# Kernel tuning notes

Measured on AMD Instinct MI355X. Metric: run time of the kernel, lower is better.

## Reference

```python
import jax, jax.numpy as jnp
import numpy as np

B, L, T, D, H, DH = 8, 1024, 1024, 768, 12, 64
SPATIAL_DIM = 5


def setup_inputs() -> dict:
    key = jax.random.key(0)
    ks = jax.random.split(key, 12)
    scale = 1.0 / np.sqrt(D)
    inp = {
        "q": jax.random.normal(ks[0], (B, L, D), dtype=jnp.float32),
        "k": jax.random.normal(ks[1], (B, T, D), dtype=jnp.float32),
        "v": jax.random.normal(ks[2], (B, T, D), dtype=jnp.float32),
        "pairwise_locs": jax.random.normal(ks[3], (B, L, T, SPATIAL_DIM), dtype=jnp.float32),
        # last 64 key positions are padding in every batch row (never all-True)
        "key_padding_mask": jnp.broadcast_to(jnp.arange(T) >= T - 64, (B, T)),
        "Wq": jax.random.normal(ks[4], (D, H * DH), dtype=jnp.float32) * scale,
        "bq": jnp.zeros((H * DH,), dtype=jnp.float32),
        "Wk": jax.random.normal(ks[5], (D, H * DH), dtype=jnp.float32) * scale,
        "bk": jnp.zeros((H * DH,), dtype=jnp.float32),
        "Wv": jax.random.normal(ks[6], (D, H * DH), dtype=jnp.float32) * scale,
        "bv": jnp.zeros((H * DH,), dtype=jnp.float32),
        "Wo": jax.random.normal(ks[7], (H * DH, D), dtype=jnp.float32) * scale,
        "bo": jnp.zeros((D,), dtype=jnp.float32),
    }
    return inp


def reference(q, k, v, pairwise_locs, key_padding_mask, Wq, bq, Wk, bk, Wv, bv, Wo, bo):
    # pairwise_locs is accepted but unused in this forward path (as in the source).
    b, l, _ = q.shape
    t = k.shape[1]
    qh = (q @ Wq + bq).reshape(b, l, H, DH)  # b l h d
    kh = (k @ Wk + bk).reshape(b, t, H, DH)  # b t h d
    vh = (v @ Wv + bv).reshape(b, t, H, DH)  # b t h d
    attn = jnp.einsum('blhd,bthd->bhlt', qh, kh) / jnp.sqrt(jnp.float32(DH))
    attn = jnp.where(key_padding_mask[:, None, None, :], -jnp.inf, attn)
    fused_attn = jax.nn.softmax(attn, axis=-1)
    out = jnp.einsum('bhlt,bthd->blhd', fused_attn, vh).reshape(b, l, H * DH)
    return out @ Wo + bo  # dropout is identity in eval mode
```

## Files before the change

### kernel.cpp

```cpp
#include <hip/hip_runtime.h>
#include <hip/hip_bf16.h>
#include <cstdint>
#include <cstddef>
#include <cmath>

#define NB 8
#define NL 1024
#define NT 1024
#define ND 768
#define NH 12
#define NDH 64
#define NM (NB*NL)

typedef short short8 __attribute__((ext_vector_type(8)));
typedef unsigned short ushort4v __attribute__((ext_vector_type(4)));
typedef unsigned int uint4v __attribute__((ext_vector_type(4)));
typedef float f32x4 __attribute__((ext_vector_type(4)));
typedef float f32x16 __attribute__((ext_vector_type(16)));
typedef float float4v __attribute__((ext_vector_type(4)));

__device__ __forceinline__ unsigned short f2bf(float f) {
  union { __hip_bfloat16 h; unsigned short u; } cv;
  cv.h = __float2bfloat16(f);
  return cv.u;
}
__device__ __forceinline__ unsigned pk2(float lo, float hi) {
  return (unsigned)f2bf(lo) | ((unsigned)f2bf(hi) << 16);
}
__device__ __forceinline__ void gll16(const void* g, void* l) {
  __builtin_amdgcn_global_load_lds(
      (const __attribute__((address_space(1))) unsigned int*)g,
      (__attribute__((address_space(3))) unsigned int*)l, 16, 0, 0);
}

__global__ __launch_bounds__(128) void maskbits_kernel(
    const unsigned int* __restrict__ mask, unsigned long long* __restrict__ mb) {
  const int id = threadIdx.x;
  const unsigned int* src = mask + (size_t)(id >> 4) * NT + (id & 15) * 64;
  unsigned long long m = 0;
  for (int j = 0; j < 64; j++) m |= (unsigned long long)(src[j] != 0u) << j;
  mb[id] = m;
}

__global__ __launch_bounds__(256) void wt_kernel(
    const float* __restrict__ W0, const float* __restrict__ W1,
    const float* __restrict__ W2, const float* __restrict__ W3,
    unsigned short* __restrict__ Wt) {
  __shared__ float tile[32][33];
  const float* W = blockIdx.z == 0 ? W0 : blockIdx.z == 1 ? W1 : blockIdx.z == 2 ? W2 : W3;
  const int k0 = blockIdx.x * 32, n0 = blockIdx.y * 32;
  const int tx = threadIdx.x & 31, ty = threadIdx.x >> 5;
  for (int r = ty; r < 32; r += 8) tile[r][tx] = W[(size_t)(k0 + r) * ND + n0 + tx];
  __syncthreads();
  unsigned short* out = Wt + (size_t)blockIdx.z * ND * ND;
  for (int r = ty; r < 32; r += 8) out[(size_t)(n0 + r) * ND + k0 + tx] = f2bf(tile[tx][r]);
}

template<int MODE>
__global__ __launch_bounds__(256) void gemm_kernel(
    const float* __restrict__ Af0, const float* __restrict__ Af1,
    const float* __restrict__ Af2, const unsigned short* __restrict__ Ab,
    const unsigned short* __restrict__ Wt,
    const float* __restrict__ bias0, const float* __restrict__ bias1,
    const float* __restrict__ bias2,
    unsigned short* __restrict__ outb0, unsigned short* __restrict__ outb1,
    unsigned short* __restrict__ outb2, float* __restrict__ outf) {
  __shared__ __align__(16) unsigned short As[128 * 64];
  __shared__ __align__(16) unsigned short Bs[128 * 64];
  const int tid = threadIdx.x, lane = tid & 63, w = tid >> 6;
  const int c = lane & 15, g = lane >> 4;
  const int wrow = w & 1, wcol = w >> 1;
  const int l8 = lane >> 3, l7 = lane & 7, csw = l7 ^ l8;
  const int mbase = blockIdx.x * 128, nbase = blockIdx.y * 128;
  const int z = (MODE == 0) ? blockIdx.z : 3;

  const float* Af = (MODE == 0) ? (z == 0 ? Af0 : z == 1 ? Af1 : Af2) : nullptr;
  const unsigned short* Bt = Wt + (size_t)z * ND * ND;
  const float* bias = (MODE == 0) ? (z == 0 ? bias0 : z == 1 ? bias1 : bias2) : bias0;

  f32x4 acc[4][4];
#pragma unroll
  for (int m = 0; m < 4; m++)
#pragma unroll
    for (int n = 0; n < 4; n++) acc[m][n] = (f32x4){0.f, 0.f, 0.f, 0.f};

  for (int k0 = 0; k0 < ND; k0 += 64) {
    if (MODE == 0) {
#pragma unroll
      for (int i = 0; i < 4; i++) {
        int id = i * 256 + tid;
        int r = id >> 3, cc = id & 7;
        const float* src = &Af[(size_t)(mbase + r) * ND + k0 + cc * 8];
        float4v x0 = *(const float4v*)src;
        float4v x1 = *(const float4v*)(src + 4);
        uint4v y = {pk2(x0[0], x0[1]), pk2(x0[2], x0[3]),
                    pk2(x1[0], x1[1]), pk2(x1[2], x1[3])};
        *(uint4v*)&As[r * 64 + ((cc ^ (r & 7)) * 8)] = y;
      }
    } else {
#pragma unroll
      for (int it = 0; it < 4; it++) {
        int r = it * 32 + w * 8 + l8;
        gll16(&Ab[(size_t)(mbase + r) * ND + k0 + csw * 8], &As[(it * 32 + w * 8) * 64]);
      }
    }
#pragma unroll
    for (int it = 0; it < 4; it++) {
      int r = it * 32 + w * 8 + l8;
      gll16(&Bt[(size_t)(nbase + r) * ND + k0 + csw * 8], &Bs[(it * 32 + w * 8) * 64]);
    }
    __syncthreads();

#pragma unroll
    for (int ks = 0; ks < 2; ks++) {
      short8 a[4], b[4];
#pragma unroll
      for (int m = 0; m < 4; m++) {
        int r = wrow * 64 + m * 16 + c;
        a[m] = *(const short8*)&As[r * 64 + (((ks * 4 + g) ^ (c & 7)) * 8)];
      }
#pragma unroll
      for (int n = 0; n < 4; n++) {
        int r = wcol * 64 + n * 16 + c;
        b[n] = *(const short8*)&Bs[r * 64 + (((ks * 4 + g) ^ (c & 7)) * 8)];
      }
      if (MODE == 0 && z == 2) {
#pragma unroll
        for (int m = 0; m < 4; m++)
#pragma unroll
          for (int n = 0; n < 4; n++)
            acc[m][n] = __builtin_amdgcn_mfma_f32_16x16x32_bf16(a[m], b[n], acc[m][n], 0, 0, 0);
      } else {
#pragma unroll
        for (int m = 0; m < 4; m++)
#pragma unroll
          for (int n = 0; n < 4; n++)
            acc[m][n] = __builtin_amdgcn_mfma_f32_16x16x32_bf16(b[n], a[m], acc[m][n], 0, 0, 0);
      }
    }
    __syncthreads();
  }

  if (MODE == 0 && z == 2) {
#pragma unroll
    for (int n = 0; n < 4; n++) {
      const int col = nbase + wcol * 64 + n * 16 + c;
      const float bv = bias[col];
      const int h = col >> 6, dd = col & 63;
#pragma unroll
      for (int m = 0; m < 4; m++) {
        const int r0 = mbase + wrow * 64 + m * 16 + g * 4;
        const int bb = r0 >> 10, t = r0 & (NT - 1);
        ushort4v y;
#pragma unroll
        for (int j = 0; j < 4; j++) y[j] = f2bf(acc[m][n][j] + bv);
        *(ushort4v*)&outb2[((size_t)(bb * NH + h) * NDH + dd) * NT + t] = y;
      }
    }
  } else {
    const float scale = (MODE == 0 && z == 0) ? 0.125f * 1.44269504f : 1.0f;
    unsigned short* outb = (MODE == 0) ? (z == 0 ? outb0 : outb1) : nullptr;
#pragma unroll
    for (int n = 0; n < 4; n++) {
      const int colb = nbase + wcol * 64 + n * 16 + g * 4;
      float4v bv4 = *(const float4v*)&bias[colb];
#pragma unroll
      for (int m = 0; m < 4; m++) {
        const int row = mbase + wrow * 64 + m * 16 + c;
        if (MODE == 3) {
          float4v y;
#pragma unroll
          for (int j = 0; j < 4; j++) y[j] = acc[m][n][j] + bv4[j];
          *(float4v*)&outf[(size_t)row * ND + colb] = y;
        } else {
          ushort4v y;
#pragma unroll
          for (int j = 0; j < 4; j++) y[j] = f2bf((acc[m][n][j] + bv4[j]) * scale);
          *(ushort4v*)&outb[(size_t)row * ND + colb] = y;
        }
      }
    }
  }
}

__global__ __launch_bounds__(256) void attn_kernel(
    const unsigned short* __restrict__ qh, const unsigned short* __restrict__ kh,
    const unsigned short* __restrict__ vhT, const unsigned long long* __restrict__ maskbits,
    unsigned short* __restrict__ ao) {
  __shared__ __align__(16) unsigned short Ks[2][64 * 64];
  __shared__ __align__(16) unsigned short Vs[2][64 * 64];
  const int tid = threadIdx.x, lane = tid & 63, w = tid >> 6;
  const int q32 = lane & 31, hi = lane >> 5;
  const int l8 = lane >> 3, l7 = lane & 7;

  const int lin = blockIdx.x;
  const int qb = ((lin >> 3) & 7) * 128;
  const int bh = (lin & 7) + 8 * (lin >> 6);
  const int b = bh / NH, h = bh % NH;
  const size_t kbase = (size_t)b * NT * ND + h * NDH;
  const size_t vbase = (size_t)(b * NH + h) * NDH * NT;

  const unsigned mwsrc = ((const unsigned*)maskbits)[(size_t)b * 32 + (lane & 31)];

  short8 aq[4];
  {
    size_t qrow = (size_t)(b * NL + qb + w * 32 + q32) * ND + h * NDH + hi * 8;
#pragma unroll
    for (int ks = 0; ks < 4; ks++)
      aq[ks] = *(const short8*)&qh[qrow + ks * 16];
  }

  f32x16 o[2] = {{}, {}};
  f32x4 lrv = {0.f, 0.f, 0.f, 0.f};
  float mr = -1e30f;

#pragma unroll
  for (int it = 0; it < 2; it++) {
    int r = w * 16 + it * 8 + l8;
    int cs = l7 ^ (r & 7);
    gll16(&kh[kbase + (size_t)r * ND + cs * 8], &Ks[0][(w * 16 + it * 8) * 64]);
    gll16(&vhT[vbase + (size_t)r * NT + cs * 8], &Vs[0][(w * 16 + it * 8) * 64]);
  }
  __syncthreads();

  for (int g0 = 0; g0 < NT; g0 += 64) {
    const int cur = (g0 >> 6) & 1;
    const int tIdx = g0 >> 6;
    if (g0 + 64 < NT) {
      unsigned nlo = __shfl(mwsrc, tIdx * 2 + 2, 64);
      unsigned nhi = __shfl(mwsrc, tIdx * 2 + 3, 64);
      if ((nlo & nhi) != 0xffffffffu) {
#pragma unroll
        for (int it = 0; it < 2; it++) {
          int r = w * 16 + it * 8 + l8;
          int cs = l7 ^ (r & 7);
          gll16(&kh[kbase + (size_t)(g0 + 64 + r) * ND + cs * 8],
                &Ks[cur ^ 1][(w * 16 + it * 8) * 64]);
          gll16(&vhT[vbase + (size_t)r * NT + (g0 + 64) + cs * 8],
                &Vs[cur ^ 1][(w * 16 + it * 8) * 64]);
        }
      }
    }

    unsigned mlo = __shfl(mwsrc, tIdx * 2, 64);
    unsigned mhi_ = __shfl(mwsrc, tIdx * 2 + 1, 64);

    if ((mlo & mhi_) != 0xffffffffu) {
      const bool anymask = (mlo | mhi_) != 0u;
#pragma unroll
      for (int tt = 0; tt < 2; tt++) {
        f32x16 s = {};
        __builtin_amdgcn_s_setprio(1);
#pragma unroll
        for (int ks = 0; ks < 4; ks++) {
          short8 ak = *(const short8*)&Ks[cur][(tt * 32 + q32) * 64 +
                          ((((ks << 1) | hi) ^ (q32 & 7)) * 8)];
          s = __builtin_amdgcn_mfma_f32_32x32x16_bf16(ak, aq[ks], s, 0, 0, 0);
        }
        __builtin_amdgcn_s_setprio(0);

        if (anymask) {
          unsigned wsd = tt ? mhi_ : mlo;
          wsd = hi ? (wsd >> 4) : wsd;
#pragma unroll
          for (int a = 0; a < 4; a++)
#pragma unroll
            for (int j = 0; j < 4; j++)
              if ((wsd >> (8 * a + j)) & 1) s[4 * a + j] = -INFINITY;
        }

        float mt = s[0];
#pragma unroll
        for (int r = 1; r < 16; r++) mt = fmaxf(mt, s[r]);
        mt = fmaxf(mt, __shfl_xor(mt, 32, 64));
        if (!__all(mt <= mr + 8.f)) {
          float mnew = fmaxf(mr, mt);
          float alpha = exp2f(mr - mnew);
          mr = mnew;
          lrv *= alpha; o[0] *= alpha; o[1] *= alpha;
        }
        unsigned pkv[4][2];
#pragma unroll
        for (int a = 0; a < 4; a++) {
          f32x4 p;
#pragma unroll
          for (int j = 0; j < 4; j++) p[j] = exp2f(s[4 * a + j] - mr);
          lrv += p;
          pkv[a][0] = pk2(p[0], p[1]);
          pkv[a][1] = pk2(p[2], p[3]);
        }

#pragma unroll
        for (int ts = 0; ts < 2; ts++) {
          unsigned u0 = pkv[2 * ts][0], u1 = pkv[2 * ts][1];
          unsigned w0 = pkv[2 * ts + 1][0], w1 = pkv[2 * ts + 1][1];
          unsigned r0 = __shfl_xor(hi ? u0 : w0, 32, 64);
          unsigned r1 = __shfl_xor(hi ? u1 : w1, 32, 64);
          union { unsigned u[4]; short8 s8; } bp;
          bp.u[0] = hi ? r0 : u0;
          bp.u[1] = hi ? r1 : u1;
          bp.u[2] = hi ? w0 : r0;
          bp.u[3] = hi ? w1 : r1;
          __builtin_amdgcn_s_setprio(1);
#pragma unroll
          for (int dt = 0; dt < 2; dt++) {
            short8 av = *(const short8*)&Vs[cur][(dt * 32 + q32) * 64 +
                            ((((tt << 2) | (ts << 1) | hi) ^ (q32 & 7)) * 8)];
            o[dt] = __builtin_amdgcn_mfma_f32_32x32x16_bf16(av, bp.s8, o[dt], 0, 0, 0);
          }
          __builtin_amdgcn_s_setprio(0);
        }
      }
    }
    __syncthreads();
  }

  float lr = (lrv[0] + lrv[1]) + (lrv[2] + lrv[3]);
  lr += __shfl_xor(lr, 32, 64);
  float inv = 1.f / lr;
  size_t row = (size_t)(b * NL + qb + w * 32 + q32) * ND + h * NDH;
#pragma unroll
  for (int dt = 0; dt < 2; dt++)
#pragma unroll
    for (int a = 0; a < 4; a++) {
      ushort4v y;
#pragma unroll
      for (int j = 0; j < 4; j++) y[j] = f2bf(o[dt][4 * a + j] * inv);
      *(ushort4v*)&ao[row + dt * 32 + 8 * a + 4 * hi] = y;
    }
}

extern "C" void kernel_launch(void* const* d_in, const int* in_sizes, int n_in,
                              void* d_out, int out_size, void* d_ws, size_t ws_size,
                              hipStream_t stream) {
  const float* q  = (const float*)d_in[0];
  const float* k  = (const float*)d_in[1];
  const float* v  = (const float*)d_in[2];
  const unsigned int* mask = (const unsigned int*)d_in[4];
  const float* Wq = (const float*)d_in[5];
  const float* bq = (const float*)d_in[6];
  const float* Wk = (const float*)d_in[7];
  const float* bk = (const float*)d_in[8];
  const float* Wv = (const float*)d_in[9];
  const float* bv = (const float*)d_in[10];
  const float* Wo = (const float*)d_in[11];
  const float* bo = (const float*)d_in[12];
  float* out = (float*)d_out;

  unsigned short* ws  = (unsigned short*)d_ws;
  unsigned short* Wt  = ws;
  unsigned short* qhb = Wt + (size_t)4 * ND * ND;
  unsigned short* khb = qhb + (size_t)NM * ND;
  unsigned short* vhT = khb + (size_t)NM * ND;
  unsigned short* aob = vhT + (size_t)NM * ND;
  unsigned long long* mb = (unsigned long long*)(aob + (size_t)NM * ND);

  wt_kernel<<<dim3(ND / 32, ND / 32, 4), 256, 0, stream>>>(Wq, Wk, Wv, Wo, Wt);
  maskbits_kernel<<<1, 128, 0, stream>>>(mask, mb);

  gemm_kernel<0><<<dim3(NM / 128, ND / 128, 3), 256, 0, stream>>>(
      q, k, v, nullptr, Wt, bq, bk, bv, qhb, khb, vhT, nullptr);

  attn_kernel<<<dim3(NL / 128 * NB * NH), 256, 0, stream>>>(qhb, khb, vhT, mb, aob);

  gemm_kernel<3><<<dim3(NM / 128, ND / 128), 256, 0, stream>>>(
      nullptr, nullptr, nullptr, aob, Wt, bo, nullptr, nullptr,
      nullptr, nullptr, nullptr, out);
}
```

Measured before the change: 156.7 us.

## Triple-buffer K/V tiles in attention with prefetch distance two and vmcnt waits

Moves the attention kernel's K/V shared-memory staging from double to triple buffering, prefetching tile t+2 while computing tile t. The full __syncthreads is replaced by explicit s_waitcnt vmcnt(4) plus s_barrier, so the loads for the next-next tile can stay in flight across the barrier. This hides more global-load latency, at the cost of 50% more LDS per block, which may reduce occupancy, and of relying on hand-counted vmcnt values.

Result: no change. 157.5 us (+0.5%).

```diff
diff --git a/kernel.cpp b/kernel.cpp
--- a/kernel.cpp
+++ b/kernel.cpp
@@ -187,8 +187,8 @@
     const unsigned short* __restrict__ qh, const unsigned short* __restrict__ kh,
     const unsigned short* __restrict__ vhT, const unsigned long long* __restrict__ maskbits,
     unsigned short* __restrict__ ao) {
-  __shared__ __align__(16) unsigned short Ks[2][64 * 64];
-  __shared__ __align__(16) unsigned short Vs[2][64 * 64];
+  __shared__ __align__(16) unsigned short Ks[3][64 * 64];
+  __shared__ __align__(16) unsigned short Vs[3][64 * 64];
   const int tid = threadIdx.x, lane = tid & 63, w = tid >> 6;
   const int q32 = lane & 31, hi = lane >> 5;
   const int l8 = lane >> 3, l7 = lane & 7;
@@ -214,36 +214,48 @@
   f32x4 lrv = {0.f, 0.f, 0.f, 0.f};
   float mr = -1e30f;
 
-#pragma unroll
-  for (int it = 0; it < 2; it++) {
-    int r = w * 16 + it * 8 + l8;
-    int cs = l7 ^ (r & 7);
-    gll16(&kh[kbase + (size_t)r * ND + cs * 8], &Ks[0][(w * 16 + it * 8) * 64]);
-    gll16(&vhT[vbase + (size_t)r * NT + cs * 8], &Vs[0][(w * 16 + it * 8) * 64]);
-  }
-  __syncthreads();
-
-  for (int g0 = 0; g0 < NT; g0 += 64) {
-    const int cur = (g0 >> 6) & 1;
-    const int tIdx = g0 >> 6;
-    if (g0 + 64 < NT) {
-      unsigned nlo = __shfl(mwsrc, tIdx * 2 + 2, 64);
-      unsigned nhi = __shfl(mwsrc, tIdx * 2 + 3, 64);
-      if ((nlo & nhi) != 0xffffffffu) {
-#pragma unroll
-        for (int it = 0; it < 2; it++) {
-          int r = w * 16 + it * 8 + l8;
-          int cs = l7 ^ (r & 7);
-          gll16(&kh[kbase + (size_t)(g0 + 64 + r) * ND + cs * 8],
-                &Ks[cur ^ 1][(w * 16 + it * 8) * 64]);
-          gll16(&vhT[vbase + (size_t)r * NT + (g0 + 64) + cs * 8],
-                &Vs[cur ^ 1][(w * 16 + it * 8) * 64]);
-        }
-      }
-    }
-
-    unsigned mlo = __shfl(mwsrc, tIdx * 2, 64);
-    unsigned mhi_ = __shfl(mwsrc, tIdx * 2 + 1, 64);
+  const int srow = w * 16 + l8;
+  const int scs0 = l7 ^ (srow & 7), scs1 = l7 ^ ((srow + 8) & 7);
+
+#define STAGE(gidx, nb)                                                        \
+  do {                                                                         \
+    gll16(&kh[kbase + (size_t)((gidx) * 64 + srow) * ND + scs0 * 8],           \
+          &Ks[nb][(w * 16) * 64]);                                             \
+    gll16(&vhT[vbase + (size_t)srow * NT + (gidx) * 64 + scs0 * 8],            \
+          &Vs[nb][(w * 16) * 64]);                                             \
+    gll16(&kh[kbase + (size_t)((gidx) * 64 + srow + 8) * ND + scs1 * 8],       \
+          &Ks[nb][(w * 16 + 8) * 64]);                                         \
+    gll16(&vhT[vbase + (size_t)(srow + 8) * NT + (gidx) * 64 + scs1 * 8],      \
+          &Vs[nb][(w * 16 + 8) * 64]);                                         \
+  } while (0)
+
+  STAGE(0, 0);
+  STAGE(1, 1);
+  asm volatile("s_waitcnt vmcnt(4)" ::: "memory");
+  __builtin_amdgcn_sched_barrier(0);
+  __builtin_amdgcn_s_barrier();
+  __builtin_amdgcn_sched_barrier(0);
+
+  int cur = 0;
+  unsigned mlo = __shfl(mwsrc, 0, 64);
+  unsigned mhi_ = __shfl(mwsrc, 1, 64);
+
+  for (int tIdx = 0; tIdx < NT / 64; tIdx++) {
+    bool issued = false;
+    if (tIdx + 2 < NT / 64) {
+      unsigned plo = __shfl(mwsrc, tIdx * 2 + 4, 64);
+      unsigned phi = __shfl(mwsrc, tIdx * 2 + 5, 64);
+      if ((plo & phi) != 0xffffffffu) {
+        int nb = cur + 2; if (nb >= 3) nb -= 3;
+        STAGE(tIdx + 2, nb);
+        issued = true;
+      }
+    }
+    unsigned nlo = 0xffffffffu, nhi = 0xffffffffu;
+    if (tIdx + 1 < NT / 64) {
+      nlo = __shfl(mwsrc, tIdx * 2 + 2, 64);
+      nhi = __shfl(mwsrc, tIdx * 2 + 3, 64);
+    }
 
     if ((mlo & mhi_) != 0xffffffffu) {
       const bool anymask = (mlo | mhi_) != 0u;
@@ -312,8 +324,19 @@
         }
       }
     }
-    __syncthreads();
+
+    if (issued)
+      asm volatile("s_waitcnt vmcnt(4) lgkmcnt(0)" ::: "memory");
+    else
+      asm volatile("s_waitcnt vmcnt(0) lgkmcnt(0)" ::: "memory");
+    __builtin_amdgcn_sched_barrier(0);
+    __builtin_amdgcn_s_barrier();
+    __builtin_amdgcn_sched_barrier(0);
+
+    mlo = nlo; mhi_ = nhi;
+    cur = (cur == 2) ? 0 : cur + 1;
   }
+#undef STAGE
 
   float lr = (lrv[0] + lrv[1]) + (lrv[2] + lrv[3]);
   lr += __shfl_xor(lr, 32, 64);
```
